# Kernel optimization log

Hardware: AMD Instinct MI355X
Metric: run time of the kernel (lower is better)

Reference implementation:

```python
import jax, jax.numpy as jnp
import numpy as np

RETURN_INDEX = 0  # return_index init kwarg
D_MODEL = 64
NUM_FEATURES = 362


def setup_inputs() -> dict:
    key = jax.random.key(0)
    k1, k2, k3, k4, k5 = jax.random.split(key, 5)
    B, S, N, F, D = 4, 128, 512, NUM_FEATURES, D_MODEL
    x = jax.random.normal(k1, (B, S, N, F), dtype=jnp.float32)
    s = 1.0 / np.sqrt(F)  # torch nn.Linear default init bound
    Wg_w = jax.random.uniform(k2, (D, F), minval=-s, maxval=s, dtype=jnp.float32)
    Wg_b = jax.random.uniform(k3, (D,), minval=-s, maxval=s, dtype=jnp.float32)
    Wh_w = jax.random.uniform(k4, (D, F), minval=-s, maxval=s, dtype=jnp.float32)
    Wh_b = jax.random.uniform(k5, (D,), minval=-s, maxval=s, dtype=jnp.float32)
    return {"x": x, "Wg_w": Wg_w, "Wg_b": Wg_b, "Wh_w": Wh_w, "Wh_b": Wh_b}


def reference(x, Wg_w, Wg_b, Wh_w, Wh_b):
    # x: [B, S, N, F]. Haar dwt -> idwt(cA,None)/idwt(None,cD) collapses to:
    #   rec_l[2k] = rec_l[2k+1] = (x[2k]+x[2k+1])/2
    #   rec_h[2k] = -rec_h[2k+1] = (x[2k]-x[2k+1])/2
    B, S, N, F = x.shape
    r = x[:, :, :, RETURN_INDEX]                      # [B, S, N]
    rp = r.reshape(B, S // 2, 2, N)                   # pair adjacent time steps
    avg = (rp[:, :, 0] + rp[:, :, 1]) * 0.5           # [B, S//2, N]
    diff = (rp[:, :, 0] - rp[:, :, 1]) * 0.5          # [B, S//2, N]
    X_l = jnp.stack([avg, avg], axis=2).reshape(B, S, N)
    X_h = jnp.stack([diff, -diff], axis=2).reshape(B, S, N)
    X_l_full = x.at[:, :, :, RETURN_INDEX].set(X_l)
    X_h_full = x.at[:, :, :, RETURN_INDEX].set(X_h)
    X_l_proj = jnp.einsum('bsnf,df->bsnd', X_l_full, Wg_w) + Wg_b
    X_h_proj = jnp.einsum('bsnf,df->bsnd', X_h_full, Wh_w) + Wh_b
    return (X_l_proj, X_h_proj)
```

## Files before the change

### kernel.cpp

```cpp
#include <hip/hip_runtime.h>
#include <hip/hip_bf16.h>
#include <stdint.h>

#define M_ROWS (4*128*512)
#define FDIM 362
#define KSTEPS 12
#define TROWS 16
#define ROWB 1448
#define TILEB (TROWS*ROWB)
#define GRID 1024
#define TPB 16
#define OUT_HALF 16777216

typedef __attribute__((ext_vector_type(8))) short bf16x8;
typedef __attribute__((ext_vector_type(4))) float f32x4;

__device__ __forceinline__ float2 ld2(const float* p) { return *(const float2*)p; }

__device__ __forceinline__ bf16x8 pack8(float2 a, float2 b, float2 c, float2 d) {
  union { __hip_bfloat162 h[4]; bf16x8 v; } t;
  t.h[0] = __float22bfloat162_rn(a);
  t.h[1] = __float22bfloat162_rn(b);
  t.h[2] = __float22bfloat162_rn(c);
  t.h[3] = __float22bfloat162_rn(d);
  return t.v;
}

__global__ __launch_bounds__(256, 2) void dfl_kernel(
    const float* __restrict__ x,
    const float* __restrict__ Wg,
    const float* __restrict__ Wgb,
    const float* __restrict__ Wh,
    const float* __restrict__ Whb,
    float* __restrict__ out)
{
  __shared__ __attribute__((aligned(16))) unsigned char Ab[2][TILEB];
  __shared__ __attribute__((aligned(16))) unsigned char tb[4*2048];

  const int tid  = threadIdx.x;
  const int lane = tid & 63;
  const int wv   = tid >> 6;
  const int q    = lane >> 4;
  const int l15  = lane & 15;
  const bool is_h = wv >= 2;
  const int colb  = (wv & 1) * 32;
  const float* Wsel  = is_h ? Wh  : Wg;
  const float* Wbsel = is_h ? Whb : Wgb;

  bf16x8 bw[2][KSTEPS];
  float biasf[2], w0f[2];
#pragma unroll
  for (int f = 0; f < 2; ++f) {
    const int dloc = colb + f*16 + l15;
    const float* wrow = Wsel + (size_t)dloc * FDIM;
    biasf[f] = Wbsel[dloc];
    w0f[f]   = wrow[0];
#pragma unroll
    for (int k = 0; k < KSTEPS; ++k) {
      float2 t0 = make_float2(0.f,0.f), t1 = t0, t2 = t0, t3 = t0;
      if (k < 11) {
        const float* p = wrow + k*32 + q*8;
        t0 = ld2(p); t1 = ld2(p+2); t2 = ld2(p+4); t3 = ld2(p+6);
      } else if (q == 0) {
        t0 = ld2(wrow+352); t1 = ld2(wrow+354); t2 = ld2(wrow+356); t3 = ld2(wrow+358);
      } else if (q == 1) {
        t0 = ld2(wrow+360);
      }
      bw[f][k] = pack8(t0, t1, t2, t3);
    }
  }

  if (tid < 6) *(f32x4*)(&Ab[1][0] + tid*16) = (f32x4){0.f,0.f,0.f,0.f};

  auto stage = [&](int tile, int p) {
    const unsigned char* src = (const unsigned char*)(x + (size_t)tile * TROWS * FDIM);
    unsigned char* dst = &Ab[p][0];
#pragma unroll
    for (int j = 0; j < 6; ++j) {
      const int chunk = wv*384 + j*64 + lane;
      if (chunk < TILEB/16) {
        __builtin_amdgcn_global_load_lds(
            (const __attribute__((address_space(1))) unsigned int*)(src + (size_t)chunk*16),
            (__attribute__((address_space(3))) unsigned int*)(dst + (wv*384 + j*64)*16),
            16, 0, 0);
      }
    }
  };

  unsigned char* wb = tb + wv*2048;
  float* outp = out + (is_h ? OUT_HALF : 0) + colb;

  stage((int)blockIdx.x, 0);
  __syncthreads();

  for (int i = 0; i < TPB; ++i) {
    const int p  = i & 1;
    const int m0 = ((int)blockIdx.x + i*GRID) * TROWS;
    if (i + 1 < TPB) stage((int)blockIdx.x + (i+1)*GRID, p ^ 1);

    float rp = 0.f;
    if (lane < 16) rp = x[(size_t)((m0 ^ 512) + l15) * FDIM];

    const unsigned char* AbP = &Ab[p][0];
    const unsigned char* ap  = AbP + l15*ROWB + q*32;

    f32x4 acc0 = {biasf[0],biasf[0],biasf[0],biasf[0]};
    f32x4 acc1 = {biasf[1],biasf[1],biasf[1],biasf[1]};
#pragma unroll
    for (int k = 0; k < KSTEPS; ++k) {
      const unsigned char* pk = ap + k*128;
      float2 f0 = *(const float2*)(pk);
      float2 f1 = *(const float2*)(pk + 8);
      float2 f2 = *(const float2*)(pk + 16);
      float2 f3 = *(const float2*)(pk + 24);
      bf16x8 av = pack8(f0, f1, f2, f3);
      acc0 = __builtin_amdgcn_mfma_f32_16x16x32_bf16(av, bw[0][k], acc0, 0,0,0);
      acc1 = __builtin_amdgcn_mfma_f32_16x16x32_bf16(av, bw[1][k], acc1, 0,0,0);
    }

    const float rs = *(const float*)(AbP + l15*ROWB);
    const float cval = is_h ? -(rs + rp)*0.5f : (rp - rs)*0.5f;

#pragma unroll
    for (int jj = 0; jj < 4; ++jj) {
      const float cc = __shfl(cval, q*4 + jj, 64);
      const int rl = q*4 + jj;
#pragma unroll
      for (int fn = 0; fn < 2; ++fn) {
        const float v = (fn ? acc1[jj] : acc0[jj]) + cc * w0f[fn];
        const int col = fn*16 + l15;
        const int boff = rl*128 + ((((col>>2) ^ (rl&7))) << 4) + ((col&3) << 2);
        *(float*)(wb + boff) = v;
      }
    }
#pragma unroll
    for (int s = 0; s < 2; ++s) {
      const int rr = s*8 + (lane >> 3);
      const int cs = lane & 7;
      f32x4 vv = *(const f32x4*)(wb + rr*128 + (((cs ^ (rr&7))) << 4));
      *(f32x4*)(outp + (size_t)(m0 + rr)*64 + cs*4) = vv;
    }

    __syncthreads();
  }
}

extern "C" void kernel_launch(void* const* d_in, const int* in_sizes, int n_in,
                              void* d_out, int out_size, void* d_ws, size_t ws_size,
                              hipStream_t stream) {
  (void)in_sizes; (void)n_in; (void)d_ws; (void)ws_size; (void)out_size;
  const float* x   = (const float*)d_in[0];
  const float* Wg  = (const float*)d_in[1];
  const float* Wgb = (const float*)d_in[2];
  const float* Wh  = (const float*)d_in[3];
  const float* Whb = (const float*)d_in[4];
  float* out = (float*)d_out;
  dfl_kernel<<<GRID, 256, 0, stream>>>(x, Wg, Wgb, Wh, Whb, out);
}
```

Baseline: 116.3 us.

## Triple-buffer async LDS tile loads with explicit vmcnt waits instead of syncthreads

Moves from double to triple buffering of the x tiles in LDS, prefetching two tiles ahead with global_load_lds. The full __syncthreads is replaced by hand-tuned s_waitcnt vmcnt counts plus s_barrier, and sched_barriers pin the instruction order. Staging is rebalanced so each wave loads an equal share of the chunks, and the tail k-step reads only valid columns rather than relying on zero padding. This is meant to hide global load latency better, at the cost of more LDS per block, which may lower occupancy, and fragile hard-coded wait counts.

Result: no change. 117.2 us (+0.8%).

```diff
diff --git a/kernel.cpp b/kernel.cpp
--- a/kernel.cpp
+++ b/kernel.cpp
@@ -4,10 +4,10 @@
 
 #define M_ROWS (4*128*512)
 #define FDIM 362
-#define KSTEPS 12
 #define TROWS 16
 #define ROWB 1448
 #define TILEB (TROWS*ROWB)
+#define CPW 362
 #define GRID 1024
 #define TPB 16
 #define OUT_HALF 16777216
@@ -15,7 +15,7 @@
 typedef __attribute__((ext_vector_type(8))) short bf16x8;
 typedef __attribute__((ext_vector_type(4))) float f32x4;
 
-__device__ __forceinline__ float2 ld2(const float* p) { return *(const float2*)p; }
+template<int N> struct Ic { static constexpr int value = N; };
 
 __device__ __forceinline__ bf16x8 pack8(float2 a, float2 b, float2 c, float2 d) {
   union { __hip_bfloat162 h[4]; bf16x8 v; } t;
@@ -25,6 +25,7 @@
   t.h[3] = __float22bfloat162_rn(d);
   return t.v;
 }
+__device__ __forceinline__ float2 ld2(const float* p) { return *(const float2*)p; }
 
 __global__ __launch_bounds__(256, 2) void dfl_kernel(
     const float* __restrict__ x,
@@ -34,7 +35,7 @@
     const float* __restrict__ Whb,
     float* __restrict__ out)
 {
-  __shared__ __attribute__((aligned(16))) unsigned char Ab[2][TILEB];
+  __shared__ __attribute__((aligned(16))) unsigned char Ab[3][TILEB];
   __shared__ __attribute__((aligned(16))) unsigned char tb[4*2048];
 
   const int tid  = threadIdx.x;
@@ -47,7 +48,7 @@
   const float* Wsel  = is_h ? Wh  : Wg;
   const float* Wbsel = is_h ? Whb : Wgb;
 
-  bf16x8 bw[2][KSTEPS];
+  bf16x8 bw[2][12];
   float biasf[2], w0f[2];
 #pragma unroll
   for (int f = 0; f < 2; ++f) {
@@ -56,7 +57,7 @@
     biasf[f] = Wbsel[dloc];
     w0f[f]   = wrow[0];
 #pragma unroll
-    for (int k = 0; k < KSTEPS; ++k) {
+    for (int k = 0; k < 12; ++k) {
       float2 t0 = make_float2(0.f,0.f), t1 = t0, t2 = t0, t3 = t0;
       if (k < 11) {
         const float* p = wrow + k*32 + q*8;
@@ -70,18 +71,16 @@
     }
   }
 
-  if (tid < 6) *(f32x4*)(&Ab[1][0] + tid*16) = (f32x4){0.f,0.f,0.f,0.f};
-
   auto stage = [&](int tile, int p) {
     const unsigned char* src = (const unsigned char*)(x + (size_t)tile * TROWS * FDIM);
     unsigned char* dst = &Ab[p][0];
 #pragma unroll
     for (int j = 0; j < 6; ++j) {
-      const int chunk = wv*384 + j*64 + lane;
-      if (chunk < TILEB/16) {
+      const int cbase = wv*CPW + j*64;
+      if (lane < CPW - j*64) {
         __builtin_amdgcn_global_load_lds(
-            (const __attribute__((address_space(1))) unsigned int*)(src + (size_t)chunk*16),
-            (__attribute__((address_space(3))) unsigned int*)(dst + (wv*384 + j*64)*16),
+            (const __attribute__((address_space(1))) unsigned int*)(src + (size_t)(cbase + lane)*16),
+            (__attribute__((address_space(3))) unsigned int*)(dst + cbase*16),
             16, 0, 0);
       }
     }
@@ -90,32 +89,40 @@
   unsigned char* wb = tb + wv*2048;
   float* outp = out + (is_h ? OUT_HALF : 0) + colb;
 
-  stage((int)blockIdx.x, 0);
-  __syncthreads();
+  auto round = [&](int i, auto sflag, auto wc) {
+    const int p  = i % 3;
+    const int m0 = ((int)blockIdx.x + i*GRID) * TROWS;
 
-  for (int i = 0; i < TPB; ++i) {
-    const int p  = i & 1;
-    const int m0 = ((int)blockIdx.x + i*GRID) * TROWS;
-    if (i + 1 < TPB) stage((int)blockIdx.x + (i+1)*GRID, p ^ 1);
-
-    float rp = 0.f;
-    if (lane < 16) rp = x[(size_t)((m0 ^ 512) + l15) * FDIM];
+    const float rp = x[(size_t)((m0 ^ 512) + l15) * FDIM];
+    __builtin_amdgcn_sched_barrier(0);
+    if constexpr (decltype(sflag)::value)
+      stage((int)blockIdx.x + (i+2)*GRID, (i+2) % 3);
+    __builtin_amdgcn_sched_barrier(0);
 
     const unsigned char* AbP = &Ab[p][0];
     const unsigned char* ap  = AbP + l15*ROWB + q*32;
-
     f32x4 acc0 = {biasf[0],biasf[0],biasf[0],biasf[0]};
     f32x4 acc1 = {biasf[1],biasf[1],biasf[1],biasf[1]};
 #pragma unroll
-    for (int k = 0; k < KSTEPS; ++k) {
+    for (int k = 0; k < 11; ++k) {
       const unsigned char* pk = ap + k*128;
-      float2 f0 = *(const float2*)(pk);
-      float2 f1 = *(const float2*)(pk + 8);
-      float2 f2 = *(const float2*)(pk + 16);
-      float2 f3 = *(const float2*)(pk + 24);
-      bf16x8 av = pack8(f0, f1, f2, f3);
+      bf16x8 av = pack8(*(const float2*)pk, *(const float2*)(pk+8),
+                        *(const float2*)(pk+16), *(const float2*)(pk+24));
       acc0 = __builtin_amdgcn_mfma_f32_16x16x32_bf16(av, bw[0][k], acc0, 0,0,0);
       acc1 = __builtin_amdgcn_mfma_f32_16x16x32_bf16(av, bw[1][k], acc1, 0,0,0);
+    }
+    {
+      const unsigned char* pk = ap + 11*128;
+      float2 z2 = make_float2(0.f,0.f), f0 = z2, f1 = z2, f2 = z2, f3 = z2;
+      if (q == 0) {
+        f0 = *(const float2*)pk;      f1 = *(const float2*)(pk+8);
+        f2 = *(const float2*)(pk+16); f3 = *(const float2*)(pk+24);
+      } else if (q == 1) {
+        f0 = *(const float2*)pk;
+      }
+      bf16x8 av = pack8(f0, f1, f2, f3);
+      acc0 = __builtin_amdgcn_mfma_f32_16x16x32_bf16(av, bw[0][11], acc0, 0,0,0);
+      acc1 = __builtin_amdgcn_mfma_f32_16x16x32_bf16(av, bw[1][11], acc1, 0,0,0);
     }
 
     const float rs = *(const float*)(AbP + l15*ROWB);
@@ -141,8 +148,27 @@
       *(f32x4*)(outp + (size_t)(m0 + rr)*64 + cs*4) = vv;
     }
 
-    __syncthreads();
-  }
+    __builtin_amdgcn_sched_barrier(0);
+    if constexpr (decltype(wc)::value >= 0) {
+      asm volatile("s_waitcnt vmcnt(%0)" :: "i"(decltype(wc)::value) : "memory");
+      __builtin_amdgcn_s_barrier();
+    }
+    __builtin_amdgcn_sched_barrier(0);
+  };
+
+  __builtin_amdgcn_sched_barrier(0);
+  asm volatile("s_waitcnt vmcnt(0)" ::: "memory");
+  stage((int)blockIdx.x, 0);
+  stage((int)blockIdx.x + GRID, 1);
+  __builtin_amdgcn_sched_barrier(0);
+  asm volatile("s_waitcnt vmcnt(6)" ::: "memory");
+  __builtin_amdgcn_s_barrier();
+  __builtin_amdgcn_sched_barrier(0);
+
+  round(0, Ic<1>{}, Ic<9>{});
+  for (int i = 1; i <= 13; ++i) round(i, Ic<1>{}, Ic<11>{});
+  round(14, Ic<0>{}, Ic<5>{});
+  round(15, Ic<0>{}, Ic<-1>{});
 }
 
 extern "C" void kernel_launch(void* const* d_in, const int* in_sizes, int n_in,
```
